# Performance work log

Hardware: AMD Instinct MI355X
Metric: run time of the kernel (lower is better)

## Reference

```python
import jax, jax.numpy as jnp
import numpy as np

N_NODES = 100000
N_EDGES = 1600000
IN_C, HID_C, OUT_C = 256, 128, 64


def setup_inputs() -> dict:
    key = jax.random.key(0)
    k_x, k_e, k_w1, k_w2 = jax.random.split(key, 4)
    x = jax.random.normal(k_x, (N_NODES, IN_C), dtype=jnp.float32)
    edge_index = jax.random.randint(k_e, (2, N_EDGES), 0, N_NODES, dtype=jnp.int64)
    # Glorot-ish init scaled like PyG defaults
    W1 = jax.random.normal(k_w1, (IN_C, HID_C), dtype=jnp.float32) * (1.0 / np.sqrt(IN_C))
    b1 = jnp.zeros((HID_C,), dtype=jnp.float32)
    W2 = jax.random.normal(k_w2, (HID_C, OUT_C), dtype=jnp.float32) * (1.0 / np.sqrt(HID_C))
    b2 = jnp.zeros((OUT_C,), dtype=jnp.float32)
    return {"x": x, "edge_index": edge_index, "W1": W1, "b1": b1, "W2": W2, "b2": b2}


def _gcn_norm(edge_index, n_nodes, dtype):
    # PyG gcn_norm: add self-loops, deg over targets, norm = d_i^-1/2 * d_j^-1/2
    loop = jnp.arange(n_nodes, dtype=edge_index.dtype)
    src = jnp.concatenate([edge_index[0], loop])
    dst = jnp.concatenate([edge_index[1], loop])
    deg = jax.ops.segment_sum(jnp.ones_like(dst, dtype=dtype), dst, num_segments=n_nodes)
    dis = jnp.where(deg > 0, jax.lax.rsqrt(jnp.maximum(deg, 1e-12)), 0.0).astype(dtype)
    norm = dis[src] * dis[dst]  # [E + N]
    return src, dst, norm


def _gcn_conv(x, src, dst, norm, W, b, n_nodes):
    h = x @ W                                    # [N, C_out] dense transform first
    msg = h[src] * norm[:, None]                 # edge-wise gather + scale
    agg = jax.ops.segment_sum(msg, dst, num_segments=n_nodes)  # scatter-add
    return agg + b


def reference(x, edge_index, W1, b1, W2, b2):
    n = x.shape[0]
    src, dst, norm = _gcn_norm(edge_index, n, x.dtype)
    h = _gcn_conv(x, src, dst, norm, W1, b1, n)
    out = _gcn_conv(h, src, dst, norm, W2, b2, n)
    return out
```

## Files before the change

kernel.cpp:

```cpp
#include <hip/hip_runtime.h>
#include <math.h>

#define IN_C  256
#define HID_C 128
#define OUT_C 64
#define CHUNK 4096
#define MAXNB 400

typedef short bf16x8 __attribute__((ext_vector_type(8)));
typedef float f32x4  __attribute__((ext_vector_type(4)));

__device__ __forceinline__ unsigned short f2bf(float f) {
    unsigned u = __float_as_uint(f);
    unsigned rounding = 0x7FFFu + ((u >> 16) & 1u);
    return (unsigned short)((u + rounding) >> 16);
}

__global__ void detect_kernel(const void* edges, int E, int n_nodes, int* flag) {
    if (threadIdx.x == 0 && blockIdx.x == 0) {
        const long long* p = (const long long*)edges;
        int k = E < 64 ? E : 64;
        int is64 = 1;
        for (int i = 0; i < k; ++i) {
            long long v = p[i];
            if (v < 0 || v >= n_nodes) { is64 = 0; break; }
        }
        *flag = is64;
    }
}

__device__ __forceinline__ int load_edge(const void* edges, size_t idx, int is64) {
    return is64 ? (int)((const long long*)edges)[idx] : ((const int*)edges)[idx];
}

__global__ void convert_wt(const float* __restrict__ W, unsigned short* __restrict__ Wt,
                           int K, int N) {
    int idx = blockIdx.x * 256 + threadIdx.x;
    if (idx >= K * N) return;
    int k = idx / N, n_ = idx % N;
    Wt[(size_t)n_ * K + k] = f2bf(W[idx]);
}

__global__ __launch_bounds__(1024) void conv_hist(
    const float* __restrict__ x, unsigned short* __restrict__ xb, int nconv,
    const void* edges, const int* __restrict__ flag,
    int* __restrict__ hist, int E, int NB, int CH, int CONV) {
    __shared__ int h[MAXNB];
    const int bid = blockIdx.x;
    if (bid < CONV) {
        int t = bid * 1024 + threadIdx.x;
        int stride = CONV * 1024;
        for (int i = t; i < nconv; i += stride) {
            const float4* p = (const float4*)(x + (size_t)i * 8);
            float4 a = p[0], b = p[1];
            union { unsigned short u[8]; uint4 v; } t8;
            t8.u[0] = f2bf(a.x); t8.u[1] = f2bf(a.y); t8.u[2] = f2bf(a.z); t8.u[3] = f2bf(a.w);
            t8.u[4] = f2bf(b.x); t8.u[5] = f2bf(b.y); t8.u[6] = f2bf(b.z); t8.u[7] = f2bf(b.w);
            *(uint4*)(xb + (size_t)i * 8) = t8.v;
        }
        return;
    }
    const int c = bid - CONV;
    for (int b = threadIdx.x; b < NB; b += 1024) h[b] = 0;
    __syncthreads();
    const int f = *flag;
    const int e0 = c * CHUNK + threadIdx.x;
    #pragma unroll
    for (int k = 0; k < CHUNK / 1024; ++k) {
        int e = e0 + k * 1024;
        if (e < E) {
            int d = load_edge(edges, (size_t)E + e, f);
            atomicAdd(&h[d >> 8], 1);
        }
    }
    __syncthreads();
    for (int b = threadIdx.x; b < NB; b += 1024)
        hist[(size_t)b * CH + c] = h[b];
}

__global__ __launch_bounds__(512) void scan_chunks(
    int* __restrict__ hist, int* __restrict__ bucketTotal, int NB, int CH) {
    __shared__ int tmp[512];
    const int b = blockIdx.x;
    const int t = threadIdx.x;
    int v = (t < CH) ? hist[(size_t)b * CH + t] : 0;
    tmp[t] = v;
    __syncthreads();
    for (int off = 1; off < 512; off <<= 1) {
        int u = (t >= off) ? tmp[t - off] : 0;
        __syncthreads();
        if (t >= off) tmp[t] += u;
        __syncthreads();
    }
    if (t < CH) hist[(size_t)b * CH + t] = tmp[t] - v;
    if (t == 511) bucketTotal[b] = tmp[511];
}

__global__ __launch_bounds__(512) void scan_buckets(int* __restrict__ base, int NB, int Etot) {
    __shared__ int tmp[512];
    const int t = threadIdx.x;
    int v = (t < NB) ? base[t] : 0;
    tmp[t] = v;
    __syncthreads();
    for (int off = 1; off < 512; off <<= 1) {
        int u = (t >= off) ? tmp[t - off] : 0;
        __syncthreads();
        if (t >= off) tmp[t] += u;
        __syncthreads();
    }
    if (t < NB) base[t] = tmp[t] - v;
    if (t == 0) base[NB] = Etot;
}

__global__ __launch_bounds__(1024) void partition_edges(
    const void* edges, const int* __restrict__ flag,
    const int* __restrict__ chunkBase, const int* __restrict__ bucketBase,
    unsigned* __restrict__ epart, int E, int NB, int CH) {
    __shared__ int cur[MAXNB];
    const int c = blockIdx.x;
    for (int b = threadIdx.x; b < NB; b += 1024)
        cur[b] = chunkBase[(size_t)b * CH + c] + bucketBase[b];
    __syncthreads();
    const int f = *flag;
    const int e0 = c * CHUNK + threadIdx.x;
    #pragma unroll
    for (int k = 0; k < CHUNK / 1024; ++k) {
        int e = e0 + k * 1024;
        if (e < E) {
            int d = load_edge(edges, (size_t)E + e, f);
            int s = load_edge(edges, e, f);
            int pos = atomicAdd(&cur[d >> 8], 1);
            epart[pos] = (unsigned)s | ((unsigned)(d & 255) << 24);
        }
    }
}

__global__ __launch_bounds__(256) void bucket_sort(
    const unsigned* __restrict__ epart, const int* __restrict__ bucketBase,
    int* __restrict__ ssrc, int* __restrict__ deg, int* __restrict__ row_ptr,
    float* __restrict__ dis, int n) {
    __shared__ int cnt[256];
    __shared__ int tmp[256];
    __shared__ int cursor[256];
    const int b = blockIdx.x;
    const int t = threadIdx.x;
    const int bstart = bucketBase[b], bend = bucketBase[b + 1];
    cnt[t] = 0;
    __syncthreads();
    for (int i = bstart + t; i < bend; i += 256)
        atomicAdd(&cnt[epart[i] >> 24], 1);
    __syncthreads();
    int v = cnt[t];
    tmp[t] = v;
    __syncthreads();
    for (int off = 1; off < 256; off <<= 1) {
        int u = (t >= off) ? tmp[t - off] : 0;
        __syncthreads();
        if (t >= off) tmp[t] += u;
        __syncthreads();
    }
    int excl = tmp[t] - v;
    cursor[t] = excl;
    int node = b * 256 + t;
    if (node < n) {
        deg[node] = v;
        row_ptr[node] = bstart + excl;
        dis[node] = rsqrtf((float)v + 1.0f);
    }
    __syncthreads();
    for (int i = bstart + t; i < bend; i += 256) {
        unsigned p = epart[i];
        int pos = bstart + atomicAdd(&cursor[p >> 24], 1);
        ssrc[pos] = (int)(p & 0xFFFFFFu);
    }
}

template<int TN, int K>
__global__ __launch_bounds__(256) void gemm_mfma_bb(
    const unsigned short* __restrict__ A, const unsigned short* __restrict__ Wt,
    const float* __restrict__ dis, unsigned short* __restrict__ C, int M) {
    constexpr int TM = 64, KC = 64, NCF = TN / 16;
    __shared__ __align__(16) unsigned short A_lds[TM * KC];
    __shared__ __align__(16) unsigned short B_lds[TN * KC];
    const int tid  = threadIdx.x;
    const int wave = tid >> 6;
    const int lane = tid & 63;
    const int q    = lane >> 4;
    const int cl   = lane & 15;
    const long long row0 = (long long)blockIdx.x * TM;

    f32x4 acc[NCF];
    const f32x4 fzero = {0.f, 0.f, 0.f, 0.f};
    #pragma unroll
    for (int cf = 0; cf < NCF; ++cf) acc[cf] = fzero;

    for (int k0 = 0; k0 < K; k0 += KC) {
        #pragma unroll
        for (int p = 0; p < 2; ++p) {
            int i = p * 256 + tid;
            int r = i >> 3, c = i & 7;
            uint4 v = *(const uint4*)(A + (row0 + r) * K + k0 + c * 8);
            *(uint4*)((char*)A_lds + r * 128 + ((c ^ (r & 7)) * 16)) = v;
        }
        #pragma unroll
        for (int p = 0; p < TN / 32; ++p) {
            int i = p * 256 + tid;
            int bc = i >> 3, c = i & 7;
            uint4 v = *(const uint4*)(Wt + (size_t)bc * K + k0 + c * 8);
            *(uint4*)((char*)B_lds + bc * 128 + ((c ^ (bc & 7)) * 16)) = v;
        }
        __syncthreads();
        #pragma unroll
        for (int ksub = 0; ksub < 2; ++ksub) {
            const int cidx = ksub * 4 + q;
            const int r = wave * 16 + cl;
            bf16x8 af = *(const bf16x8*)((const char*)A_lds + r * 128 + ((cidx ^ (r & 7)) * 16));
            #pragma unroll
            for (int cf = 0; cf < NCF; ++cf) {
                const int bc = cf * 16 + cl;
                bf16x8 bfr = *(const bf16x8*)((const char*)B_lds + bc * 128 + ((cidx ^ (bc & 7)) * 16));
                acc[cf] = __builtin_amdgcn_mfma_f32_16x16x32_bf16(af, bfr, acc[cf], 0, 0, 0);
            }
        }
        __syncthreads();
    }
    #pragma unroll
    for (int j = 0; j < 4; ++j) {
        long long row = row0 + wave * 16 + q * 4 + j;
        if (row >= M) continue;
        float d = dis[row];
        #pragma unroll
        for (int cf = 0; cf < NCF; ++cf)
            C[row * TN + cf * 16 + cl] = f2bf(acc[cf][j] * d);
    }
}

template<int C, int NPB, bool OBF>
__global__ __launch_bounds__(256) void gather_layer_bf(
    const unsigned short* __restrict__ hs, const int* __restrict__ row_ptr,
    const int* __restrict__ deg, const int* __restrict__ ssrc,
    const float* __restrict__ dis, const float* __restrict__ bias,
    void* __restrict__ outp, int n) {
    constexpr int TPN = C / 8;
    const int local = threadIdx.x / TPN;
    const int lane  = threadIdx.x % TPN;
    const int i = blockIdx.x * NPB + local;
    if (i >= n) return;
    const uint4* h4 = (const uint4*)hs;
    float di = dis[i];
    float acc[8] = {};
    auto accum = [&](uint4 u) {
        acc[0] += __uint_as_float(u.x << 16);
        acc[1] += __uint_as_float(u.x & 0xffff0000u);
        acc[2] += __uint_as_float(u.y << 16);
        acc[3] += __uint_as_float(u.y & 0xffff0000u);
        acc[4] += __uint_as_float(u.z << 16);
        acc[5] += __uint_as_float(u.z & 0xffff0000u);
        acc[6] += __uint_as_float(u.w << 16);
        acc[7] += __uint_as_float(u.w & 0xffff0000u);
    };
    accum(h4[(size_t)i * TPN + lane]);
    const int start = row_ptr[i];
    const int cnt   = deg[i];
    const int* sp = ssrc + start;
    int j = 0;
    for (; j + 8 <= cnt; j += 8) {
        uint4 v[8];
        #pragma unroll
        for (int k = 0; k < 8; ++k) v[k] = h4[(size_t)sp[j + k] * TPN + lane];
        #pragma unroll
        for (int k = 0; k < 8; ++k) accum(v[k]);
    }
    for (; j + 4 <= cnt; j += 4) {
        uint4 v[4];
        #pragma unroll
        for (int k = 0; k < 4; ++k) v[k] = h4[(size_t)sp[j + k] * TPN + lane];
        #pragma unroll
        for (int k = 0; k < 4; ++k) accum(v[k]);
    }
    for (; j < cnt; ++j) accum(h4[(size_t)sp[j] * TPN + lane]);
    const float* bp = bias + lane * 8;
    float o[8];
    #pragma unroll
    for (int k = 0; k < 8; ++k) o[k] = bp[k] + di * acc[k];
    if constexpr (OBF) {
        union { unsigned short u[8]; uint4 v; } t8;
        #pragma unroll
        for (int k = 0; k < 8; ++k) t8.u[k] = f2bf(o[k]);
        *(uint4*)((unsigned short*)outp + (size_t)i * C + lane * 8) = t8.v;
    } else {
        float* op = (float*)outp + (size_t)i * C + lane * 8;
        *(float4*)op = make_float4(o[0], o[1], o[2], o[3]);
        *(float4*)(op + 4) = make_float4(o[4], o[5], o[6], o[7]);
    }
}

extern "C" void kernel_launch(void* const* d_in, const int* in_sizes, int n_in,
                              void* d_out, int out_size, void* d_ws, size_t ws_size,
                              hipStream_t stream) {
    const float* x     = (const float*)d_in[0];
    const void*  edges = d_in[1];
    const float* W1    = (const float*)d_in[2];
    const float* b1    = (const float*)d_in[3];
    const float* W2    = (const float*)d_in[4];
    const float* b2    = (const float*)d_in[5];
    float* out = (float*)d_out;

    const int n  = in_sizes[0] / IN_C;
    const int E  = in_sizes[1] / 2;
    const int NB = (n + 255) / 256;
    const int CH = (E + CHUNK - 1) / CHUNK;

    char* ws = (char*)d_ws;
    size_t off = 0;
    auto alloc = [&](size_t bytes) { char* p = ws + off; off += (bytes + 255) & ~(size_t)255; return p; };
    int*   flag       = (int*)  alloc(4);
    int*   hist       = (int*)  alloc((size_t)NB * CH * 4);
    int*   bucketBase = (int*)  alloc((size_t)(NB + 1) * 4);
    int*   deg        = (int*)  alloc((size_t)n * 4);
    int*   row_ptr    = (int*)  alloc((size_t)n * 4);
    float* dis        = (float*)alloc((size_t)n * 4);
    unsigned* epart   = (unsigned*)alloc((size_t)E * 4);
    int*   ssrc       = (int*)  alloc((size_t)E * 4);
    unsigned short* xb   = (unsigned short*)alloc((size_t)(n + 64) * IN_C * 2);
    unsigned short* hs   = (unsigned short*)alloc((size_t)(n + 64) * HID_C * 2);
    unsigned short* aggb = (unsigned short*)alloc((size_t)(n + 64) * HID_C * 2);
    unsigned short* Wt1  = (unsigned short*)alloc((size_t)IN_C * HID_C * 2);
    unsigned short* Wt2  = (unsigned short*)alloc((size_t)HID_C * OUT_C * 2);

    detect_kernel<<<1, 64, 0, stream>>>(edges, E, n, flag);
    convert_wt<<<(IN_C * HID_C + 255) / 256, 256, 0, stream>>>(W1, Wt1, IN_C, HID_C);
    convert_wt<<<(HID_C * OUT_C + 255) / 256, 256, 0, stream>>>(W2, Wt2, HID_C, OUT_C);

    const int CONV = 256;
    const int nconv = n * IN_C / 8;
    conv_hist<<<CONV + CH, 1024, 0, stream>>>(x, xb, nconv, edges, flag, hist, E, NB, CH, CONV);

    scan_chunks<<<NB, 512, 0, stream>>>(hist, bucketBase, NB, CH);
    scan_buckets<<<1, 512, 0, stream>>>(bucketBase, NB, E);

    partition_edges<<<CH, 1024, 0, stream>>>(edges, flag, hist, bucketBase, epart, E, NB, CH);
    bucket_sort<<<NB, 256, 0, stream>>>(epart, bucketBase, ssrc, deg, row_ptr, dis, n);

    gemm_mfma_bb<HID_C, IN_C><<<(n + 63) / 64, 256, 0, stream>>>(xb, Wt1, dis, hs, n);
    gather_layer_bf<HID_C, 16, true><<<(n + 15) / 16, 256, 0, stream>>>(hs, row_ptr, deg, ssrc, dis, b1, aggb, n);

    gemm_mfma_bb<OUT_C, HID_C><<<(n + 63) / 64, 256, 0, stream>>>(aggb, Wt2, dis, hs, n);
    gather_layer_bf<OUT_C, 32, false><<<(n + 31) / 32, 256, 0, stream>>>(hs, row_ptr, deg, ssrc, dis, b2, out, n);
}
```

Measured before the change: 200.9 us.

## Pre-sort bucket edges by source range in LDS before destination sort

Each bucket's packed edges are loaded into shared memory and counting-sorted by source ID (in 1024-node groups) before the per-destination counting sort. Because the final scatter preserves that partial source order within each destination row, the later gather of h[src] should see better locality. The cost is an extra pass over epart, more LDS per block (about 24KB), and a fallback to the old path when a bucket exceeds capacity. Atomic order makes the source ordering only approximate.

```diff
diff --git a/kernel.cpp b/kernel.cpp
--- a/kernel.cpp
+++ b/kernel.cpp
@@ -6,6 +6,7 @@
 #define OUT_C 64
 #define CHUNK 4096
 #define MAXNB 400
+#define LDSCAP 6144
 
 typedef short bf16x8 __attribute__((ext_vector_type(8)));
 typedef float f32x4  __attribute__((ext_vector_type(4)));
@@ -139,16 +140,48 @@
     const unsigned* __restrict__ epart, const int* __restrict__ bucketBase,
     int* __restrict__ ssrc, int* __restrict__ deg, int* __restrict__ row_ptr,
     float* __restrict__ dis, int n) {
+    __shared__ unsigned sbuf[LDSCAP];
+    __shared__ int scnt[128];
     __shared__ int cnt[256];
     __shared__ int tmp[256];
     __shared__ int cursor[256];
     const int b = blockIdx.x;
     const int t = threadIdx.x;
     const int bstart = bucketBase[b], bend = bucketBase[b + 1];
+    const int len = bend - bstart;
+    const bool fits = (len <= LDSCAP);
+
+    if (fits) {
+        if (t < 128) scnt[t] = 0;
+        __syncthreads();
+        for (int i = t; i < len; i += 256)
+            atomicAdd(&scnt[(epart[bstart + i] & 0xFFFFFFu) >> 10], 1);
+        __syncthreads();
+        int sv = 0;
+        if (t < 128) { sv = scnt[t]; tmp[t] = sv; }
+        __syncthreads();
+        for (int off = 1; off < 128; off <<= 1) {
+            int u = (t >= off && t < 128) ? tmp[t - off] : 0;
+            __syncthreads();
+            if (t >= off && t < 128) tmp[t] += u;
+            __syncthreads();
+        }
+        if (t < 128) scnt[t] = tmp[t] - sv;
+        __syncthreads();
+        for (int i = t; i < len; i += 256) {
+            unsigned p = epart[bstart + i];
+            int pos = atomicAdd(&scnt[(p & 0xFFFFFFu) >> 10], 1);
+            sbuf[pos] = p;
+        }
+        __syncthreads();
+    }
+
     cnt[t] = 0;
     __syncthreads();
-    for (int i = bstart + t; i < bend; i += 256)
-        atomicAdd(&cnt[epart[i] >> 24], 1);
+    for (int i = t; i < len; i += 256) {
+        unsigned p = fits ? sbuf[i] : epart[bstart + i];
+        atomicAdd(&cnt[p >> 24], 1);
+    }
     __syncthreads();
     int v = cnt[t];
     tmp[t] = v;
@@ -168,8 +201,8 @@
         dis[node] = rsqrtf((float)v + 1.0f);
     }
     __syncthreads();
-    for (int i = bstart + t; i < bend; i += 256) {
-        unsigned p = epart[i];
+    for (int i = t; i < len; i += 256) {
+        unsigned p = fits ? sbuf[i] : epart[bstart + i];
         int pos = bstart + atomicAdd(&cursor[p >> 24], 1);
         ssrc[pos] = (int)(p & 0xFFFFFFu);
     }
```

Result: no change. 202.9 us (+1.0%).

## Store hidden features in column slabs so gathers hit a cache-sized slice

Applied to the files above, without the earlier changes.

The GEMM outputs are now written in a slab-major layout: 16-column slabs for layer 1 and 8-column slabs for layer 2. Each gather block processes a single slab for a range of nodes, with the slab index taken from the low bits of blockIdx. This keeps the random-gather working set for concurrently running blocks small, aiming for better L2/MALL hit rates. Neighbor index loads become nontemporal, and the second GEMM reads its A operand from the slabbed layout. The cost is that every block re-reads the CSR indices once per slab, and each gather row fetches only 16–32 bytes, so accesses are less coalesced.

```diff
diff --git a/kernel.cpp b/kernel.cpp
--- a/kernel.cpp
+++ b/kernel.cpp
@@ -176,9 +176,9 @@
 }
 
 template<int TN, int K>
-__global__ __launch_bounds__(256) void gemm_mfma_bb(
+__global__ __launch_bounds__(256) void gemm1_mfma(
     const unsigned short* __restrict__ A, const unsigned short* __restrict__ Wt,
-    const float* __restrict__ dis, unsigned short* __restrict__ C, int M) {
+    const float* __restrict__ dis, unsigned short* __restrict__ C, int M, int npad) {
     constexpr int TM = 64, KC = 64, NCF = TN / 16;
     __shared__ __align__(16) unsigned short A_lds[TM * KC];
     __shared__ __align__(16) unsigned short B_lds[TN * KC];
@@ -231,22 +231,88 @@
         float d = dis[row];
         #pragma unroll
         for (int cf = 0; cf < NCF; ++cf)
-            C[row * TN + cf * 16 + cl] = f2bf(acc[cf][j] * d);
-    }
-}
-
-template<int C, int NPB, bool OBF>
-__global__ __launch_bounds__(256) void gather_layer_bf(
-    const unsigned short* __restrict__ hs, const int* __restrict__ row_ptr,
+            C[(size_t)cf * npad * 16 + row * 16 + cl] = f2bf(acc[cf][j] * d);
+    }
+}
+
+template<int TN, int K>
+__global__ __launch_bounds__(256) void gemm2_mfma(
+    const unsigned short* __restrict__ A, const unsigned short* __restrict__ Wt,
+    const float* __restrict__ dis, unsigned short* __restrict__ C, int M, int npad) {
+    constexpr int TM = 64, KC = 64, NCF = TN / 16;
+    __shared__ __align__(16) unsigned short A_lds[TM * KC];
+    __shared__ __align__(16) unsigned short B_lds[TN * KC];
+    const int tid  = threadIdx.x;
+    const int wave = tid >> 6;
+    const int lane = tid & 63;
+    const int q    = lane >> 4;
+    const int cl   = lane & 15;
+    const long long row0 = (long long)blockIdx.x * TM;
+
+    f32x4 acc[NCF];
+    const f32x4 fzero = {0.f, 0.f, 0.f, 0.f};
+    #pragma unroll
+    for (int cf = 0; cf < NCF; ++cf) acc[cf] = fzero;
+
+    for (int k0 = 0; k0 < K; k0 += KC) {
+        #pragma unroll
+        for (int p = 0; p < 2; ++p) {
+            int i = p * 256 + tid;
+            int r = i >> 3, c = i & 7;
+            int kg = (k0 >> 3) + c;
+            uint4 v = *(const uint4*)(A + (size_t)(kg >> 1) * npad * 16
+                                        + (row0 + r) * 16 + (kg & 1) * 8);
+            *(uint4*)((char*)A_lds + r * 128 + ((c ^ (r & 7)) * 16)) = v;
+        }
+        #pragma unroll
+        for (int p = 0; p < TN / 32; ++p) {
+            int i = p * 256 + tid;
+            int bc = i >> 3, c = i & 7;
+            uint4 v = *(const uint4*)(Wt + (size_t)bc * K + k0 + c * 8);
+            *(uint4*)((char*)B_lds + bc * 128 + ((c ^ (bc & 7)) * 16)) = v;
+        }
+        __syncthreads();
+        #pragma unroll
+        for (int ksub = 0; ksub < 2; ++ksub) {
+            const int cidx = ksub * 4 + q;
+            const int r = wave * 16 + cl;
+            bf16x8 af = *(const bf16x8*)((const char*)A_lds + r * 128 + ((cidx ^ (r & 7)) * 16));
+            #pragma unroll
+            for (int cf = 0; cf < NCF; ++cf) {
+                const int bc = cf * 16 + cl;
+                bf16x8 bfr = *(const bf16x8*)((const char*)B_lds + bc * 128 + ((cidx ^ (bc & 7)) * 16));
+                acc[cf] = __builtin_amdgcn_mfma_f32_16x16x32_bf16(af, bfr, acc[cf], 0, 0, 0);
+            }
+        }
+        __syncthreads();
+    }
+    #pragma unroll
+    for (int j = 0; j < 4; ++j) {
+        long long row = row0 + wave * 16 + q * 4 + j;
+        if (row >= M) continue;
+        float d = dis[row];
+        #pragma unroll
+        for (int cf = 0; cf < NCF; ++cf) {
+            int c = cf * 16 + cl;
+            C[(size_t)(c >> 3) * npad * 8 + row * 8 + (c & 7)] = f2bf(acc[cf][j] * d);
+        }
+    }
+}
+
+template<int CPS, bool OBF>
+__global__ __launch_bounds__(256) void gather_slab(
+    const unsigned short* __restrict__ hsb, const int* __restrict__ row_ptr,
     const int* __restrict__ deg, const int* __restrict__ ssrc,
     const float* __restrict__ dis, const float* __restrict__ bias,
-    void* __restrict__ outp, int n) {
-    constexpr int TPN = C / 8;
+    void* __restrict__ outp, int n, int npad) {
+    constexpr int TPN = CPS / 8;
+    constexpr int NPB = 256 / TPN;
+    const int slab  = blockIdx.x & 7;
     const int local = threadIdx.x / TPN;
     const int lane  = threadIdx.x % TPN;
-    const int i = blockIdx.x * NPB + local;
+    const int i = (blockIdx.x >> 3) * NPB + local;
     if (i >= n) return;
-    const uint4* h4 = (const uint4*)hs;
+    const uint4* h4 = (const uint4*)(hsb + (size_t)slab * npad * CPS) ;
     float di = dis[i];
     float acc[8] = {};
     auto accum = [&](uint4 u) {
@@ -265,21 +331,20 @@
     const int* sp = ssrc + start;
     int j = 0;
     for (; j + 8 <= cnt; j += 8) {
+        int s[8];
+        #pragma unroll
+        for (int k = 0; k < 8; ++k) s[k] = __builtin_nontemporal_load(sp + j + k);
         uint4 v[8];
         #pragma unroll
-        for (int k = 0; k < 8; ++k) v[k] = h4[(size_t)sp[j + k] * TPN + lane];
+        for (int k = 0; k < 8; ++k) v[k] = h4[(size_t)s[k] * TPN + lane];
         #pragma unroll
         for (int k = 0; k < 8; ++k) accum(v[k]);
     }
-    for (; j + 4 <= cnt; j += 4) {
-        uint4 v[4];
-        #pragma unroll
-        for (int k = 0; k < 4; ++k) v[k] = h4[(size_t)sp[j + k] * TPN + lane];
-        #pragma unroll
-        for (int k = 0; k < 4; ++k) accum(v[k]);
-    }
-    for (; j < cnt; ++j) accum(h4[(size_t)sp[j] * TPN + lane]);
-    const float* bp = bias + lane * 8;
+    for (; j < cnt; ++j) {
+        int s = __builtin_nontemporal_load(sp + j);
+        accum(h4[(size_t)s * TPN + lane]);
+    }
+    const float* bp = bias + slab * CPS + lane * 8;
     float o[8];
     #pragma unroll
     for (int k = 0; k < 8; ++k) o[k] = bp[k] + di * acc[k];
@@ -287,9 +352,10 @@
         union { unsigned short u[8]; uint4 v; } t8;
         #pragma unroll
         for (int k = 0; k < 8; ++k) t8.u[k] = f2bf(o[k]);
-        *(uint4*)((unsigned short*)outp + (size_t)i * C + lane * 8) = t8.v;
+        *(uint4*)((unsigned short*)outp + (size_t)slab * npad * CPS
+                  + (size_t)i * CPS + lane * 8) = t8.v;
     } else {
-        float* op = (float*)outp + (size_t)i * C + lane * 8;
+        float* op = (float*)outp + (size_t)i * OUT_C + slab * 8;
         *(float4*)op = make_float4(o[0], o[1], o[2], o[3]);
         *(float4*)(op + 4) = make_float4(o[4], o[5], o[6], o[7]);
     }
@@ -310,6 +376,7 @@
     const int E  = in_sizes[1] / 2;
     const int NB = (n + 255) / 256;
     const int CH = (E + CHUNK - 1) / CHUNK;
+    const int npad = n + 64;
 
     char* ws = (char*)d_ws;
     size_t off = 0;
@@ -322,9 +389,9 @@
     float* dis        = (float*)alloc((size_t)n * 4);
     unsigned* epart   = (unsigned*)alloc((size_t)E * 4);
     int*   ssrc       = (int*)  alloc((size_t)E * 4);
-    unsigned short* xb   = (unsigned short*)alloc((size_t)(n + 64) * IN_C * 2);
-    unsigned short* hs   = (unsigned short*)alloc((size_t)(n + 64) * HID_C * 2);
-    unsigned short* aggb = (unsigned short*)alloc((size_t)(n + 64) * HID_C * 2);
+    unsigned short* xb   = (unsigned short*)alloc((size_t)npad * IN_C * 2);
+    unsigned short* hs   = (unsigned short*)alloc((size_t)npad * HID_C * 2);
+    unsigned short* aggb = (unsigned short*)alloc((size_t)npad * HID_C * 2);
     unsigned short* Wt1  = (unsigned short*)alloc((size_t)IN_C * HID_C * 2);
     unsigned short* Wt2  = (unsigned short*)alloc((size_t)HID_C * OUT_C * 2);
 
@@ -342,9 +409,17 @@
     partition_edges<<<CH, 1024, 0, stream>>>(edges, flag, hist, bucketBase, epart, E, NB, CH);
     bucket_sort<<<NB, 256, 0, stream>>>(epart, bucketBase, ssrc, deg, row_ptr, dis, n);
 
-    gemm_mfma_bb<HID_C, IN_C><<<(n + 63) / 64, 256, 0, stream>>>(xb, Wt1, dis, hs, n);
-    gather_layer_bf<HID_C, 16, true><<<(n + 15) / 16, 256, 0, stream>>>(hs, row_ptr, deg, ssrc, dis, b1, aggb, n);
-
-    gemm_mfma_bb<OUT_C, HID_C><<<(n + 63) / 64, 256, 0, stream>>>(aggb, Wt2, dis, hs, n);
-    gather_layer_bf<OUT_C, 32, false><<<(n + 31) / 32, 256, 0, stream>>>(hs, row_ptr, deg, ssrc, dis, b2, out, n);
-}
+    gemm1_mfma<HID_C, IN_C><<<(n + 63) / 64, 256, 0, stream>>>(xb, Wt1, dis, hs, n, npad);
+    {
+        const int ranges = (n + 127) / 128;
+        gather_slab<16, true><<<ranges * 8, 256, 0, stream>>>(
+            hs, row_ptr, deg, ssrc, dis, b1, aggb, n, npad);
+    }
+
+    gemm2_mfma<OUT_C, HID_C><<<(n + 63) / 64, 256, 0, stream>>>(aggb, Wt2, dis, hs, n, npad);
+    {
+        const int ranges = (n + 255) / 256;
+        gather_slab<8, false><<<ranges * 8, 256, 0, stream>>>(
+            hs, row_ptr, deg, ssrc, dis, b2, out, n, npad);
+    }
+}
```

Result: slower. 372.7 us (+85.5%).

## Sort nodes by degree for gather load balance and use nontemporal index loads

Applied to the files above, without the earlier changes.

Adds a counting sort of nodes by in-degree (histogram, scan, scatter) that produces a permutation, which both gather kernels use to process nodes of similar degree together. This is meant to reduce divergence between node groups within a wave that have different neighbour counts. Edge index loads become nontemporal and the 4-wide remainder loop is removed. The costs are three extra small kernels and a memset, scattered output writes and dis/row_ptr reads under the permutation, and lost locality of the node's own row.

```diff
diff --git a/kernel.cpp b/kernel.cpp
--- a/kernel.cpp
+++ b/kernel.cpp
@@ -175,6 +175,44 @@
     }
 }
 
+__global__ void deg_hist(const int* __restrict__ deg, int* __restrict__ dhist, int n) {
+    __shared__ int h[256];
+    h[threadIdx.x] = 0;
+    __syncthreads();
+    int t = blockIdx.x * 256 + threadIdx.x;
+    int stride = gridDim.x * 256;
+    for (int i = t; i < n; i += stride) {
+        int d = deg[i]; if (d > 255) d = 255;
+        atomicAdd(&h[d], 1);
+    }
+    __syncthreads();
+    if (h[threadIdx.x]) atomicAdd(&dhist[threadIdx.x], h[threadIdx.x]);
+}
+
+__global__ void deg_scan(int* __restrict__ dhist) {
+    __shared__ int tmp[256];
+    const int t = threadIdx.x;
+    int v = dhist[t];
+    tmp[t] = v;
+    __syncthreads();
+    for (int off = 1; off < 256; off <<= 1) {
+        int u = (t >= off) ? tmp[t - off] : 0;
+        __syncthreads();
+        if (t >= off) tmp[t] += u;
+        __syncthreads();
+    }
+    dhist[t] = tmp[t] - v;
+}
+
+__global__ void deg_scatter(const int* __restrict__ deg, int* __restrict__ dcur,
+                            int* __restrict__ perm, int n) {
+    int i = blockIdx.x * 256 + threadIdx.x;
+    if (i >= n) return;
+    int d = deg[i]; if (d > 255) d = 255;
+    int pos = atomicAdd(&dcur[d], 1);
+    perm[pos] = i;
+}
+
 template<int TN, int K>
 __global__ __launch_bounds__(256) void gemm_mfma_bb(
     const unsigned short* __restrict__ A, const unsigned short* __restrict__ Wt,
@@ -239,13 +277,15 @@
 __global__ __launch_bounds__(256) void gather_layer_bf(
     const unsigned short* __restrict__ hs, const int* __restrict__ row_ptr,
     const int* __restrict__ deg, const int* __restrict__ ssrc,
+    const int* __restrict__ perm,
     const float* __restrict__ dis, const float* __restrict__ bias,
     void* __restrict__ outp, int n) {
     constexpr int TPN = C / 8;
     const int local = threadIdx.x / TPN;
     const int lane  = threadIdx.x % TPN;
-    const int i = blockIdx.x * NPB + local;
-    if (i >= n) return;
+    const int ii = blockIdx.x * NPB + local;
+    if (ii >= n) return;
+    const int i = perm[ii];
     const uint4* h4 = (const uint4*)hs;
     float di = dis[i];
     float acc[8] = {};
@@ -265,20 +305,19 @@
     const int* sp = ssrc + start;
     int j = 0;
     for (; j + 8 <= cnt; j += 8) {
+        int s[8];
+        #pragma unroll
+        for (int k = 0; k < 8; ++k) s[k] = __builtin_nontemporal_load(sp + j + k);
         uint4 v[8];
         #pragma unroll
-        for (int k = 0; k < 8; ++k) v[k] = h4[(size_t)sp[j + k] * TPN + lane];
+        for (int k = 0; k < 8; ++k) v[k] = h4[(size_t)s[k] * TPN + lane];
         #pragma unroll
         for (int k = 0; k < 8; ++k) accum(v[k]);
     }
-    for (; j + 4 <= cnt; j += 4) {
-        uint4 v[4];
-        #pragma unroll
-        for (int k = 0; k < 4; ++k) v[k] = h4[(size_t)sp[j + k] * TPN + lane];
-        #pragma unroll
-        for (int k = 0; k < 4; ++k) accum(v[k]);
-    }
-    for (; j < cnt; ++j) accum(h4[(size_t)sp[j] * TPN + lane]);
+    for (; j < cnt; ++j) {
+        int s = __builtin_nontemporal_load(sp + j);
+        accum(h4[(size_t)s * TPN + lane]);
+    }
     const float* bp = bias + lane * 8;
     float o[8];
     #pragma unroll
@@ -317,8 +356,10 @@
     int*   flag       = (int*)  alloc(4);
     int*   hist       = (int*)  alloc((size_t)NB * CH * 4);
     int*   bucketBase = (int*)  alloc((size_t)(NB + 1) * 4);
+    int*   dhist      = (int*)  alloc(256 * 4);
     int*   deg        = (int*)  alloc((size_t)n * 4);
     int*   row_ptr    = (int*)  alloc((size_t)n * 4);
+    int*   perm       = (int*)  alloc((size_t)n * 4);
     float* dis        = (float*)alloc((size_t)n * 4);
     unsigned* epart   = (unsigned*)alloc((size_t)E * 4);
     int*   ssrc       = (int*)  alloc((size_t)E * 4);
@@ -331,6 +372,7 @@
     detect_kernel<<<1, 64, 0, stream>>>(edges, E, n, flag);
     convert_wt<<<(IN_C * HID_C + 255) / 256, 256, 0, stream>>>(W1, Wt1, IN_C, HID_C);
     convert_wt<<<(HID_C * OUT_C + 255) / 256, 256, 0, stream>>>(W2, Wt2, HID_C, OUT_C);
+    hipMemsetAsync(dhist, 0, 256 * 4, stream);
 
     const int CONV = 256;
     const int nconv = n * IN_C / 8;
@@ -342,9 +384,15 @@
     partition_edges<<<CH, 1024, 0, stream>>>(edges, flag, hist, bucketBase, epart, E, NB, CH);
     bucket_sort<<<NB, 256, 0, stream>>>(epart, bucketBase, ssrc, deg, row_ptr, dis, n);
 
+    deg_hist<<<128, 256, 0, stream>>>(deg, dhist, n);
+    deg_scan<<<1, 256, 0, stream>>>(dhist);
+    deg_scatter<<<(n + 255) / 256, 256, 0, stream>>>(deg, dhist, perm, n);
+
     gemm_mfma_bb<HID_C, IN_C><<<(n + 63) / 64, 256, 0, stream>>>(xb, Wt1, dis, hs, n);
-    gather_layer_bf<HID_C, 16, true><<<(n + 15) / 16, 256, 0, stream>>>(hs, row_ptr, deg, ssrc, dis, b1, aggb, n);
+    gather_layer_bf<HID_C, 16, true><<<(n + 15) / 16, 256, 0, stream>>>(
+        hs, row_ptr, deg, ssrc, perm, dis, b1, aggb, n);
 
     gemm_mfma_bb<OUT_C, HID_C><<<(n + 63) / 64, 256, 0, stream>>>(aggb, Wt2, dis, hs, n);
-    gather_layer_bf<OUT_C, 32, false><<<(n + 31) / 32, 256, 0, stream>>>(hs, row_ptr, deg, ssrc, dis, b2, out, n);
-}
+    gather_layer_bf<OUT_C, 32, false><<<(n + 31) / 32, 256, 0, stream>>>(
+        hs, row_ptr, deg, ssrc, perm, dis, b2, out, n);
+}
```

Measured after the change: 492.6 us. 2.45x slower.
